# Optimization experiments

Hardware: AMD Instinct MI355X
Metric: run time of the kernel (lower is better)

## Reference

```python
import jax, jax.numpy as jnp
import numpy as np

H, W = 512, 512
G = 8192
ALPHA_THRESH = 1.0 / 255.0        # meta_f32[0]
TRANS_THRESH = 1.0e-4             # meta_f32[1]
ALPHA_CAP = 0.99                  # meta_f32[6]
BG = jnp.zeros((3,), dtype=jnp.float32)  # config.background


def setup_inputs() -> dict:
    key = jax.random.key(0)
    ks = jax.random.split(key, 7)
    mx = jax.random.uniform(ks[0], (G,), minval=0.0, maxval=float(W))
    my = jax.random.uniform(ks[1], (G,), minval=0.0, maxval=float(H))
    means2d = jnp.stack([mx, my], axis=-1)
    # Build valid conics (inverse 2x2 covariances) from random rotation + scales
    theta = jax.random.uniform(ks[2], (G,), minval=0.0, maxval=2.0 * np.pi)
    s = jax.random.uniform(ks[3], (G, 2), minval=2.0, maxval=12.0)  # px stddevs
    ct, st = jnp.cos(theta), jnp.sin(theta)
    v1, v2 = s[:, 0] ** 2, s[:, 1] ** 2
    ca = ct * ct * v1 + st * st * v2
    cb = ct * st * (v1 - v2)
    cc = st * st * v1 + ct * ct * v2
    det = ca * cc - cb * cb
    conics = jnp.stack([cc / det, -cb / det, ca / det], axis=-1)  # [G,3] = (a,b,c)
    colors = jax.random.uniform(ks[4], (G, 3))
    opacities = jax.random.uniform(ks[5], (G,))
    depths = jax.random.uniform(ks[6], (G,), minval=0.1, maxval=100.0)
    return {"means2d": means2d, "conics": conics, "colors": colors,
            "opacities": opacities, "depths": depths}


def reference(means2d, conics, colors, opacities, depths):
    # Stable front-to-back depth sort (mirrors perm = argsort(depths, stable))
    perm = jnp.argsort(depths, stable=True)
    m = means2d[perm]
    cn = conics[perm]
    col = colors[perm]
    op = opacities[perm]
    a, b, c = cn[:, 0], cn[:, 1], cn[:, 2]
    px = jnp.arange(W, dtype=means2d.dtype) + 0.5  # pixel centers

    def row(y):
        py = y.astype(means2d.dtype) + 0.5
        dx = px[:, None] - m[None, :, 0]          # [W,G]
        dy = py - m[:, 1]                          # [G]
        sigma = 0.5 * (a * dx * dx + c * dy * dy) + b * dx * dy  # [W,G]
        alpha = jnp.minimum(ALPHA_CAP, op * jnp.exp(-sigma))
        alpha = jnp.where((sigma < 0) | (alpha < ALPHA_THRESH), 0.0, alpha)
        # exclusive cumulative transmittance along depth order
        Tprev = jnp.cumprod(1.0 - alpha, axis=-1)
        Tprev = jnp.concatenate([jnp.ones((W, 1), alpha.dtype), Tprev[:, :-1]], axis=-1)
        # early-termination: splats seen after T drops below threshold contribute 0
        wgt = alpha * Tprev * (Tprev >= TRANS_THRESH)  # [W,G]
        rgb = wgt @ col                                 # [W,3]
        t_rem = 1.0 - wgt.sum(axis=-1)                  # remaining transmittance
        return rgb + t_rem[:, None] * BG

    return jax.lax.map(row, jnp.arange(H))  # [H,W,3]
```

## Files before the change

kernel.cpp:

```cpp
#include <hip/hip_runtime.h>

#define G 8192
#define IMG_W 512
#define IMG_H 512
#define TILE 16
#define NTX (IMG_W / TILE)
#define NTY (IMG_H / TILE)
#define BLK 256
#define CAP 1024
#define ALPHA_THRESH (1.0f/255.0f)
#define ALPHA_CAP 0.99f
#define TRANS_THRESH 1e-4f

__global__ __launch_bounds__(BLK)
void range_kernel(const float* __restrict__ means2d,
                  const float* __restrict__ conics,
                  const float* __restrict__ opac,
                  unsigned int* __restrict__ ranges)
{
    int g = blockIdx.x * BLK + threadIdx.x;
    if (g >= G) return;
    float op = opac[g];
    unsigned int packed = 0xFFu;
    if (op * 255.0f >= 1.0f) {
        float smax = __logf(op * 255.0f);
        float a = conics[3*g], b = conics[3*g+1], c = conics[3*g+2];
        float det = fmaxf(a * c - b * b, 1e-12f);
        float rx = sqrtf(fmaxf(2.0f * smax * c / det, 0.0f)) * 1.0001f + 0.01f;
        float ry = sqrtf(fmaxf(2.0f * smax * a / det, 0.0f)) * 1.0001f + 0.01f;
        float mx = means2d[2*g], my = means2d[2*g+1];
        int txmin = (int)ceilf ((mx - rx - 15.5f) * 0.0625f);
        int txmax = (int)floorf((mx + rx -  0.5f) * 0.0625f);
        int tymin = (int)ceilf ((my - ry - 15.5f) * 0.0625f);
        int tymax = (int)floorf((my + ry -  0.5f) * 0.0625f);
        if (!(txmax < 0 || txmin > NTX-1 || tymax < 0 || tymin > NTY-1 ||
              txmin > txmax || tymin > tymax)) {
            txmin = max(txmin, 0); txmax = min(txmax, NTX-1);
            tymin = max(tymin, 0); tymax = min(tymax, NTY-1);
            packed = (unsigned)txmin | ((unsigned)txmax << 8)
                   | ((unsigned)tymin << 16) | ((unsigned)tymax << 24);
        }
    }
    ranges[g] = packed;
}

__device__ __forceinline__ int hitp(unsigned p, unsigned btx, unsigned bty)
{
    return (btx >= (p & 0xffu)) & (btx <= ((p >> 8) & 0xffu)) &
           (bty >= ((p >> 16) & 0xffu)) & (bty <= (p >> 24));
}

__device__ __forceinline__ float rl(float v, int l)
{
    return __uint_as_float(__builtin_amdgcn_readlane(__float_as_uint(v),
                                                     (unsigned)l));
}

__global__ __launch_bounds__(BLK)
void tile_kernel(const unsigned int* __restrict__ ranges,
                 const float* __restrict__ depths,
                 const float* __restrict__ means2d,
                 const float* __restrict__ conics,
                 const float* __restrict__ colors,
                 const float* __restrict__ opac,
                 float*       __restrict__ out)
{
    __shared__ unsigned short slist[CAP];
    __shared__ unsigned int   fkeys[CAP];
    __shared__ int woff[4];

    const int tx = threadIdx.x, ty = threadIdx.y;
    const int t = ty * TILE + tx;
    const int lane = t & 63, w = t >> 6;
    const unsigned btx = blockIdx.x, bty = blockIdx.y;

    const uint4* r4 = (const uint4*)ranges;
    const int wbase = w * (G / 4);
    uint4 rv[8];
    #pragma unroll
    for (int i = 0; i < 8; ++i)
        rv[i] = r4[(wbase >> 2) + i * 64 + lane];

    int cnt = 0;
    #pragma unroll
    for (int i = 0; i < 8; ++i)
        cnt += hitp(rv[i].x, btx, bty) + hitp(rv[i].y, btx, bty)
             + hitp(rv[i].z, btx, bty) + hitp(rv[i].w, btx, bty);
    #pragma unroll
    for (int d = 1; d < 64; d <<= 1) cnt += __shfl_xor(cnt, d);
    if (lane == 0) woff[w] = cnt;
    __syncthreads();

    int offs = 0;
    for (int ww = 0; ww < w; ++ww) offs += woff[ww];
    const int N = min(woff[0] + woff[1] + woff[2] + woff[3], CAP);

    const unsigned long long lt = (1ull << lane) - 1ull;
    #pragma unroll
    for (int i = 0; i < 8; ++i) {
        int gbase = wbase + i * 256 + lane * 4;
        int h0 = hitp(rv[i].x, btx, bty), h1 = hitp(rv[i].y, btx, bty);
        int h2 = hitp(rv[i].z, btx, bty), h3 = hitp(rv[i].w, btx, bty);
        unsigned long long m0 = __ballot(h0), m1 = __ballot(h1);
        unsigned long long m2 = __ballot(h2), m3 = __ballot(h3);
        int pos = offs + __popcll(m0 & lt) + __popcll(m1 & lt)
                       + __popcll(m2 & lt) + __popcll(m3 & lt);
        if (h0) { if (pos < CAP) slist[pos] = (unsigned short)(gbase    ); pos++; }
        if (h1) { if (pos < CAP) slist[pos] = (unsigned short)(gbase + 1); pos++; }
        if (h2) { if (pos < CAP) slist[pos] = (unsigned short)(gbase + 2); pos++; }
        if (h3) { if (pos < CAP) slist[pos] = (unsigned short)(gbase + 3); pos++; }
        offs += __popcll(m0) + __popcll(m1) + __popcll(m2) + __popcll(m3);
    }
    __syncthreads();

    unsigned short myidx[4]; unsigned int mykey[4]; int myr[4];
    #pragma unroll
    for (int m = 0; m < 4; ++m) {
        int i = t + m * BLK;
        if (i < N) {
            unsigned idx = slist[i];
            unsigned k = __float_as_uint(depths[idx]);
            myidx[m] = (unsigned short)idx; mykey[m] = k; fkeys[i] = k;
        }
    }
    __syncthreads();
    #pragma unroll
    for (int m = 0; m < 4; ++m) {
        int i = t + m * BLK;
        if (i < N) {
            unsigned ke = mykey[m]; int r = 0;
            #pragma unroll 4
            for (int j = 0; j < N; ++j) {
                unsigned kj = fkeys[j];
                r += (int)((kj < ke) | ((kj == ke) & (j < i)));
            }
            myr[m] = r;
        }
    }
    __syncthreads();
    #pragma unroll
    for (int m = 0; m < 4; ++m) {
        int i = t + m * BLK;
        if (i < N) slist[myr[m]] = myidx[m];
    }
    __syncthreads();

    const float px = (float)(btx * TILE + tx) + 0.5f;
    const float py = (float)(bty * TILE + ty) + 0.5f;
    float T = 1.0f, accr = 0.0f, accg = 0.0f, accb = 0.0f;

    for (int base = 0; base < N; base += 64) {
        int nn = min(64, N - base);
        int ll = (lane < nn) ? lane : 0;
        int idx = slist[base + ll];
        float mx = means2d[2*idx], my = means2d[2*idx+1];
        float ha = conics[3*idx]   * 0.5f;
        float hb = conics[3*idx+1];
        float hc = conics[3*idx+2] * 0.5f;
        float op = (lane < nn) ? opac[idx] : 0.0f;
        float cr = colors[3*idx], cg = colors[3*idx+1], cbl = colors[3*idx+2];

        int nn4 = (nn + 3) & ~3;
        bool fin = false;
        for (int j = 0; j < nn4; j += 4) {
            #pragma unroll
            for (int u = 0; u < 4; ++u) {
                int l = j + u;
                float smx = rl(mx, l), smy = rl(my, l);
                float sa  = rl(ha, l), sb  = rl(hb, l), sc = rl(hc, l);
                float sop = rl(op, l);
                float dx = px - smx, dy = py - smy;
                float sig = fmaf(sa, dx*dx, fmaf(sc, dy*dy, sb * (dx*dy)));
                float al = sop * __expf(-sig);
                bool ok = (sig >= 0.0f) && (al >= ALPHA_THRESH);
                al = ok ? fminf(al, ALPHA_CAP) : 0.0f;
                float wgt = al * T;
                accr = fmaf(wgt, rl(cr, l),  accr);
                accg = fmaf(wgt, rl(cg, l),  accg);
                accb = fmaf(wgt, rl(cbl, l), accb);
                T *= (1.0f - al);
            }
            if (__all(T < TRANS_THRESH)) { fin = true; break; }
        }
        if (fin) break;
    }

    const int o = (((int)bty * TILE + ty) * IMG_W + (int)btx * TILE + tx) * 3;
    out[o]     = accr;
    out[o + 1] = accg;
    out[o + 2] = accb;
}

extern "C" void kernel_launch(void* const* d_in, const int* in_sizes, int n_in,
                              void* d_out, int out_size, void* d_ws, size_t ws_size,
                              hipStream_t stream)
{
    const float* means2d = (const float*)d_in[0];
    const float* conics  = (const float*)d_in[1];
    const float* colors  = (const float*)d_in[2];
    const float* opac    = (const float*)d_in[3];
    const float* depths  = (const float*)d_in[4];
    float* out = (float*)d_out;
    unsigned int* ranges = (unsigned int*)d_ws;

    range_kernel<<<G / BLK, BLK, 0, stream>>>(means2d, conics, opac, ranges);
    tile_kernel<<<dim3(NTX, NTY), dim3(TILE, TILE), 0, stream>>>(
        ranges, depths, means2d, conics, colors, opac, out);
}
```

Measured before the change: 103.5 us.

## Pack per-splat params into aligned table and load via scalar reads

The range kernel now writes a 64-byte-aligned per-splat record holding mean, half-conic, opacity and color, plus a zero sentinel row. The tile kernel walks the sorted list four at a time and uses readfirstlane indices so each record can be fetched with uniform scalar loads. This replaces the per-64 gather plus readlane broadcasts. The rank sort now reads keys as uint4 with padding sentinels. The cost is an extra table write and serialized per-splat scalar loads, which may add latency.

```diff
diff --git a/kernel.cpp b/kernel.cpp
--- a/kernel.cpp
+++ b/kernel.cpp
@@ -15,20 +15,33 @@
 __global__ __launch_bounds__(BLK)
 void range_kernel(const float* __restrict__ means2d,
                   const float* __restrict__ conics,
+                  const float* __restrict__ colors,
                   const float* __restrict__ opac,
-                  unsigned int* __restrict__ ranges)
+                  unsigned int* __restrict__ ranges,
+                  float* __restrict__ tbl)
 {
     int g = blockIdx.x * BLK + threadIdx.x;
     if (g >= G) return;
     float op = opac[g];
+    float a  = conics[3*g], b = conics[3*g+1], c = conics[3*g+2];
+    float mx = means2d[2*g], my = means2d[2*g+1];
+    float cr = colors[3*g], cg = colors[3*g+1], cb = colors[3*g+2];
+
+    float4* t4 = (float4*)(tbl + (g << 4));
+    t4[0] = make_float4(mx, my, 0.5f * a, b);
+    t4[1] = make_float4(0.5f * c, op, cr, cg);
+    t4[2] = make_float4(cb, 0.0f, 0.0f, 0.0f);
+    if (g == 0) {
+        float4* z = (float4*)(tbl + (G << 4));
+        z[0] = z[1] = z[2] = make_float4(0.0f, 0.0f, 0.0f, 0.0f);
+    }
+
     unsigned int packed = 0xFFu;
     if (op * 255.0f >= 1.0f) {
         float smax = __logf(op * 255.0f);
-        float a = conics[3*g], b = conics[3*g+1], c = conics[3*g+2];
         float det = fmaxf(a * c - b * b, 1e-12f);
         float rx = sqrtf(fmaxf(2.0f * smax * c / det, 0.0f)) * 1.0001f + 0.01f;
         float ry = sqrtf(fmaxf(2.0f * smax * a / det, 0.0f)) * 1.0001f + 0.01f;
-        float mx = means2d[2*g], my = means2d[2*g+1];
         int txmin = (int)ceilf ((mx - rx - 15.5f) * 0.0625f);
         int txmax = (int)floorf((mx + rx -  0.5f) * 0.0625f);
         int tymin = (int)ceilf ((my - ry - 15.5f) * 0.0625f);
@@ -50,23 +63,14 @@
            (bty >= ((p >> 16) & 0xffu)) & (bty <= (p >> 24));
 }
 
-__device__ __forceinline__ float rl(float v, int l)
-{
-    return __uint_as_float(__builtin_amdgcn_readlane(__float_as_uint(v),
-                                                     (unsigned)l));
-}
-
 __global__ __launch_bounds__(BLK)
 void tile_kernel(const unsigned int* __restrict__ ranges,
                  const float* __restrict__ depths,
-                 const float* __restrict__ means2d,
-                 const float* __restrict__ conics,
-                 const float* __restrict__ colors,
-                 const float* __restrict__ opac,
+                 const float* __restrict__ tbl,
                  float*       __restrict__ out)
 {
-    __shared__ unsigned short slist[CAP];
-    __shared__ unsigned int   fkeys[CAP];
+    __shared__ unsigned short slist[CAP + 4];
+    __shared__ __align__(16) unsigned int fkeys[CAP + 4];
     __shared__ int woff[4];
 
     const int tx = threadIdx.x, ty = threadIdx.y;
@@ -123,16 +127,22 @@
             myidx[m] = (unsigned short)idx; mykey[m] = k; fkeys[i] = k;
         }
     }
-    __syncthreads();
+    if (t < 4) fkeys[N + t] = 0xFFFFFFFFu;
+    __syncthreads();
+
+    const uint4* fk4 = (const uint4*)fkeys;
+    const int nj4 = (N + 3) >> 2;
     #pragma unroll
     for (int m = 0; m < 4; ++m) {
         int i = t + m * BLK;
         if (i < N) {
             unsigned ke = mykey[m]; int r = 0;
-            #pragma unroll 4
-            for (int j = 0; j < N; ++j) {
-                unsigned kj = fkeys[j];
-                r += (int)((kj < ke) | ((kj == ke) & (j < i)));
+            for (int j4 = 0; j4 < nj4; ++j4) {
+                uint4 kv = fk4[j4]; int j = j4 << 2;
+                r += (int)((kv.x < ke) | ((kv.x == ke) & (j     < i)));
+                r += (int)((kv.y < ke) | ((kv.y == ke) & (j + 1 < i)));
+                r += (int)((kv.z < ke) | ((kv.z == ke) & (j + 2 < i)));
+                r += (int)((kv.w < ke) | ((kv.w == ke) & (j + 3 < i)));
             }
             myr[m] = r;
         }
@@ -143,46 +153,32 @@
         int i = t + m * BLK;
         if (i < N) slist[myr[m]] = myidx[m];
     }
+    if (t < 4) slist[N + t] = (unsigned short)G;
     __syncthreads();
 
     const float px = (float)(btx * TILE + tx) + 0.5f;
     const float py = (float)(bty * TILE + ty) + 0.5f;
     float T = 1.0f, accr = 0.0f, accg = 0.0f, accb = 0.0f;
 
-    for (int base = 0; base < N; base += 64) {
-        int nn = min(64, N - base);
-        int ll = (lane < nn) ? lane : 0;
-        int idx = slist[base + ll];
-        float mx = means2d[2*idx], my = means2d[2*idx+1];
-        float ha = conics[3*idx]   * 0.5f;
-        float hb = conics[3*idx+1];
-        float hc = conics[3*idx+2] * 0.5f;
-        float op = (lane < nn) ? opac[idx] : 0.0f;
-        float cr = colors[3*idx], cg = colors[3*idx+1], cbl = colors[3*idx+2];
-
-        int nn4 = (nn + 3) & ~3;
-        bool fin = false;
-        for (int j = 0; j < nn4; j += 4) {
-            #pragma unroll
-            for (int u = 0; u < 4; ++u) {
-                int l = j + u;
-                float smx = rl(mx, l), smy = rl(my, l);
-                float sa  = rl(ha, l), sb  = rl(hb, l), sc = rl(hc, l);
-                float sop = rl(op, l);
-                float dx = px - smx, dy = py - smy;
-                float sig = fmaf(sa, dx*dx, fmaf(sc, dy*dy, sb * (dx*dy)));
-                float al = sop * __expf(-sig);
-                bool ok = (sig >= 0.0f) && (al >= ALPHA_THRESH);
-                al = ok ? fminf(al, ALPHA_CAP) : 0.0f;
-                float wgt = al * T;
-                accr = fmaf(wgt, rl(cr, l),  accr);
-                accg = fmaf(wgt, rl(cg, l),  accg);
-                accb = fmaf(wgt, rl(cbl, l), accb);
-                T *= (1.0f - al);
-            }
-            if (__all(T < TRANS_THRESH)) { fin = true; break; }
-        }
-        if (fin) break;
+    for (int base = 0; base < N; base += 4) {
+        ushort4 s4 = *(const ushort4*)&slist[base];
+        unsigned short sv[4] = { s4.x, s4.y, s4.z, s4.w };
+        #pragma unroll
+        for (int u = 0; u < 4; ++u) {
+            int idx = __builtin_amdgcn_readfirstlane((int)sv[u]);
+            const float* r = tbl + (idx << 4);
+            float dx = px - r[0], dy = py - r[1];
+            float sig = fmaf(r[2], dx*dx, fmaf(r[4], dy*dy, r[3] * (dx*dy)));
+            float al = r[5] * __expf(-sig);
+            bool ok = (sig >= 0.0f) && (al >= ALPHA_THRESH);
+            al = ok ? fminf(al, ALPHA_CAP) : 0.0f;
+            float wgt = al * T;
+            accr = fmaf(wgt, r[6], accr);
+            accg = fmaf(wgt, r[7], accg);
+            accb = fmaf(wgt, r[8], accb);
+            T *= (1.0f - al);
+        }
+        if (__all(T < TRANS_THRESH)) break;
     }
 
     const int o = (((int)bty * TILE + ty) * IMG_W + (int)btx * TILE + tx) * 3;
@@ -202,8 +198,10 @@
     const float* depths  = (const float*)d_in[4];
     float* out = (float*)d_out;
     unsigned int* ranges = (unsigned int*)d_ws;
-
-    range_kernel<<<G / BLK, BLK, 0, stream>>>(means2d, conics, opac, ranges);
+    float* tbl = (float*)((char*)d_ws + 32 * 1024);
+
+    range_kernel<<<G / BLK, BLK, 0, stream>>>(means2d, conics, colors, opac,
+                                              ranges, tbl);
     tile_kernel<<<dim3(NTX, NTY), dim3(TILE, TILE), 0, stream>>>(
-        ranges, depths, means2d, conics, colors, opac, out);
-}
+        ranges, depths, tbl, out);
+}
```

After: 94.70 us. 8.5% less time.
